# Kernel optimization log

Hardware: AMD Instinct MI355X
Metric: run time of the kernel (lower is better)

Reference implementation:

```python
import jax, jax.numpy as jnp
import numpy as np

MAX_DEPTH = 7
FEAT = 32
HIDDEN = 64
RES = 2 ** MAX_DEPTH          # 128
N_VOXELS = RES ** 3           # 2^21 = 2,097,152
BATCH = 4_194_304


def setup_inputs() -> dict:
    key = jax.random.key(0)
    k = jax.random.split(key, 5)
    positions = jax.random.uniform(k[0], (BATCH, 3), dtype=jnp.float32)  # in [0,1)
    # learned parameters (torch: randn table; Linear default-init approximated)
    table = jax.random.normal(k[1], (N_VOXELS, FEAT), dtype=jnp.float32)
    W1 = jax.random.normal(k[2], (FEAT, HIDDEN), dtype=jnp.float32) * (1.0 / np.sqrt(FEAT))
    b1 = jnp.zeros((HIDDEN,), dtype=jnp.float32)
    W2 = jax.random.normal(k[3], (HIDDEN, 4), dtype=jnp.float32) * (1.0 / np.sqrt(HIDDEN))
    b2 = jnp.zeros((4,), dtype=jnp.float32)
    return {"positions": positions, "table": table, "W1": W1, "b1": b1, "W2": W2, "b2": b2}


def reference(positions, table, W1, b1, W2, b2):
    # voxel index per axis; positions in [0,1) so trunc == floor (matches .long())
    idx = jnp.clip((positions * RES).astype(jnp.int32), 0, RES - 1)  # [B,3]
    flat = idx[..., 0] * (RES * RES) + idx[..., 1] * RES + idx[..., 2]  # [B]
    feats = table[flat]                               # irregular gather [B,FEAT]
    h = jax.nn.relu(feats @ W1 + b1)                  # [B,64]
    out = h @ W2 + b2                                 # [B,4]
    rgb = jax.nn.sigmoid(out[..., :3])                # [B,3]
    density = jax.nn.softplus(out[..., 3:4])          # [B,1]
    return rgb, density
```

## Files before the change

kernel.cpp:

```cpp
#include <hip/hip_runtime.h>
#include <hip/hip_bf16.h>

typedef __attribute__((ext_vector_type(8))) short short8;
typedef __attribute__((ext_vector_type(4))) float f32x4;

#define HID 64
#define FEATN 32

static __device__ __forceinline__ short f2bf(float f) {
    __hip_bfloat16 h = __float2bfloat16(f);
    return __builtin_bit_cast(short, h);
}

__global__ __launch_bounds__(256, 4) void plen_fused(
    const float* __restrict__ pos,
    const float* __restrict__ table,
    const float* __restrict__ W1,
    const float* __restrict__ b1,
    const float* __restrict__ W2,
    const float* __restrict__ b2,
    float* __restrict__ out,
    int batch)
{
    const int lane = threadIdx.x & 63;
    const int row  = lane & 15;
    const int g    = lane >> 4;

    short8 w1f[4];
    float bias1[4];
    float w2f[4][4];
#pragma unroll
    for (int j = 0; j < 4; ++j) {
#pragma unroll
        for (int i = 0; i < 8; ++i)
            w1f[j][i] = f2bf(W1[(g * 8 + i) * HID + j * 16 + row]);
        bias1[j] = b1[j * 16 + row];
#pragma unroll
        for (int o = 0; o < 4; ++o)
            w2f[j][o] = W2[(j * 16 + row) * 4 + o];
    }

    const int r_own = row >> 2;
    const int o_own = row & 3;
    const bool is_rgb = (o_own < 3);
    const float myb2 = b2[o_own];
    const int mult = is_rgb ? 3 : 1;
    const int coff = is_rgb ? ((4 * g + r_own) * 3 + o_own)
                            : (batch * 3 + 4 * g + r_own);

    const int wave_id = blockIdx.x * 4 + (threadIdx.x >> 6);
    const int chunk = wave_id * 256;

    for (int t = 0; t < 16; ++t) {
        const int base = chunk + t * 16;

        const float* pp = pos + (size_t)(base + row) * 3;
        const float px = pp[0], py = pp[1], pz = pp[2];
        int ix = (int)(px * 128.0f);
        int iy = (int)(py * 128.0f);
        int iz = (int)(pz * 128.0f);
        ix = min(127, max(0, ix));
        iy = min(127, max(0, iy));
        iz = min(127, max(0, iz));
        const unsigned flat = ((unsigned)ix << 14) | ((unsigned)iy << 7) | (unsigned)iz;

        const float* rp = table + (size_t)flat * FEATN + g * 8;
        const f32x4 f0 = *(const f32x4*)(rp);
        const f32x4 f1 = *(const f32x4*)(rp + 4);
        short8 afrag;
        afrag[0] = f2bf(f0[0]); afrag[1] = f2bf(f0[1]);
        afrag[2] = f2bf(f0[2]); afrag[3] = f2bf(f0[3]);
        afrag[4] = f2bf(f1[0]); afrag[5] = f2bf(f1[1]);
        afrag[6] = f2bf(f1[2]); afrag[7] = f2bf(f1[3]);

        float p[16];
#pragma unroll
        for (int j = 0; j < 4; ++j) {
            const f32x4 cinit = { bias1[j], bias1[j], bias1[j], bias1[j] };
            const f32x4 acc =
                __builtin_amdgcn_mfma_f32_16x16x32_bf16(afrag, w1f[j], cinit, 0, 0, 0);
#pragma unroll
            for (int r = 0; r < 4; ++r) {
                const float h = fmaxf(acc[r], 0.0f);
                if (j == 0) {
#pragma unroll
                    for (int o = 0; o < 4; ++o) p[r * 4 + o] = h * w2f[0][o];
                } else {
#pragma unroll
                    for (int o = 0; o < 4; ++o) p[r * 4 + o] = fmaf(h, w2f[j][o], p[r * 4 + o]);
                }
            }
        }

        float v8[8];
#pragma unroll
        for (int j = 0; j < 8; ++j) {
            const float a0 = p[2 * j], b0 = p[2 * j + 1];
            const float keep = (row & 1) ? b0 : a0;
            const float give = (row & 1) ? a0 : b0;
            v8[j] = keep + __shfl_xor(give, 1, 64);
        }
        float v4[4];
#pragma unroll
        for (int j = 0; j < 4; ++j) {
            const float a0 = v8[2 * j], b0 = v8[2 * j + 1];
            const float keep = (row & 2) ? b0 : a0;
            const float give = (row & 2) ? a0 : b0;
            v4[j] = keep + __shfl_xor(give, 2, 64);
        }
        float v2[2];
#pragma unroll
        for (int j = 0; j < 2; ++j) {
            const float a0 = v4[2 * j], b0 = v4[2 * j + 1];
            const float keep = (row & 4) ? b0 : a0;
            const float give = (row & 4) ? a0 : b0;
            v2[j] = keep + __shfl_xor(give, 4, 64);
        }
        {
            const float a0 = v2[0], b0 = v2[1];
            const float keep = (row & 8) ? b0 : a0;
            const float give = (row & 8) ? a0 : b0;
            const float v = keep + __shfl_xor(give, 8, 64) + myb2;

            float resv;
            if (is_rgb) {
                resv = __builtin_amdgcn_rcpf(1.0f + __expf(-v));
            } else {
                resv = fmaxf(v, 0.0f) + __logf(1.0f + __expf(-fabsf(v)));
            }
            __builtin_nontemporal_store(resv, out + coff + base * mult);
        }
    }
}

extern "C" void kernel_launch(void* const* d_in, const int* in_sizes, int n_in,
                              void* d_out, int out_size, void* d_ws, size_t ws_size,
                              hipStream_t stream) {
    const float* pos   = (const float*)d_in[0];
    const float* table = (const float*)d_in[1];
    const float* W1    = (const float*)d_in[2];
    const float* b1    = (const float*)d_in[3];
    const float* W2    = (const float*)d_in[4];
    const float* b2    = (const float*)d_in[5];
    float* out = (float*)d_out;

    const int batch  = in_sizes[0] / 3;
    const int blocks = batch / 1024;
    hipLaunchKernelGGL(plen_fused, dim3(blocks), dim3(256), 0, stream,
                       pos, table, W1, b1, W2, b2, out, batch);
}
```

Before: 127.4 us.

## Use MFMA for second layer and software-pipeline table gathers

Swaps the operand order of the first-layer MFMA so the hidden activations land transposed, then computes the 64->4 output layer with a 16x16x16 bf16 MFMA instead of per-lane FMAs plus a four-stage shuffle reduction. Table gathers are double-buffered, so the next tile's position load and gather are in flight while the current tile computes. The position clamp is dropped, which relies on inputs lying in [0,1). The second layer now rounds hidden activations and W2 to bf16, which reduces precision, and only one quarter of the lanes issue stores.

```diff
diff --git a/kernel.cpp b/kernel.cpp
--- a/kernel.cpp
+++ b/kernel.cpp
@@ -1,16 +1,24 @@
 #include <hip/hip_runtime.h>
 #include <hip/hip_bf16.h>
 
-typedef __attribute__((ext_vector_type(8))) short short8;
+typedef __attribute__((ext_vector_type(8))) short bs8;
+typedef __attribute__((ext_vector_type(4))) short bs4;
 typedef __attribute__((ext_vector_type(4))) float f32x4;
 
 #define HID 64
 #define FEATN 32
+#define NT 16
 
 static __device__ __forceinline__ short f2bf(float f) {
     __hip_bfloat16 h = __float2bfloat16(f);
     return __builtin_bit_cast(short, h);
 }
+
+#if defined(__HIP_DEVICE_COMPILE__)
+#define MFMA16(a, b, c) __builtin_amdgcn_mfma_f32_16x16x16bf16_1k(a, b, c, 0, 0, 0)
+#else
+#define MFMA16(a, b, c) (c)
+#endif
 
 __global__ __launch_bounds__(256, 4) void plen_fused(
     const float* __restrict__ pos,
@@ -26,110 +34,94 @@
     const int row  = lane & 15;
     const int g    = lane >> 4;
 
-    short8 w1f[4];
-    float bias1[4];
-    float w2f[4][4];
+    bs8   w1f[4];
+    f32x4 bias1v[4];
+    bs4   w2tf[4];
 #pragma unroll
     for (int j = 0; j < 4; ++j) {
 #pragma unroll
         for (int i = 0; i < 8; ++i)
             w1f[j][i] = f2bf(W1[(g * 8 + i) * HID + j * 16 + row]);
-        bias1[j] = b1[j * 16 + row];
+        bias1v[j] = *(const f32x4*)(b1 + j * 16 + g * 4);
 #pragma unroll
-        for (int o = 0; o < 4; ++o)
-            w2f[j][o] = W2[(j * 16 + row) * 4 + o];
+        for (int i = 0; i < 4; ++i)
+            w2tf[j][i] = (row < 4) ? f2bf(W2[(j * 16 + g * 4 + i) * 4 + row]) : (short)0;
     }
-
-    const int r_own = row >> 2;
-    const int o_own = row & 3;
-    const bool is_rgb = (o_own < 3);
-    const float myb2 = b2[o_own];
-    const int mult = is_rgb ? 3 : 1;
-    const int coff = is_rgb ? ((4 * g + r_own) * 3 + o_own)
-                            : (batch * 3 + 4 * g + r_own);
+    f32x4 oinit;
+    if (g == 0) oinit = *(const f32x4*)b2;
+    else        oinit = (f32x4){0.f, 0.f, 0.f, 0.f};
 
     const int wave_id = blockIdx.x * 4 + (threadIdx.x >> 6);
-    const int chunk = wave_id * 256;
+    const int chunk   = wave_id * (NT * 16);
+    const size_t dns_base = (size_t)batch * 3;
 
-    for (int t = 0; t < 16; ++t) {
-        const int base = chunk + t * 16;
+    auto loadpos = [&](int t, float& x, float& y, float& z) {
+        const int tt = t < NT ? t : NT - 1;
+        const float* pp = pos + (size_t)(chunk + tt * 16 + row) * 3;
+        x = pp[0]; y = pp[1]; z = pp[2];
+    };
+    auto issue_gather = [&](float x, float y, float z, f32x4& A, f32x4& B) {
+        const unsigned ix = (unsigned)(int)(x * 128.0f);
+        const unsigned iy = (unsigned)(int)(y * 128.0f);
+        const unsigned iz = (unsigned)(int)(z * 128.0f);
+        const unsigned flat = (ix << 14) | (iy << 7) | iz;
+        const float* rp = table + (size_t)flat * FEATN + g * 8;
+        A = *(const f32x4*)rp;
+        B = *(const f32x4*)(rp + 4);
+    };
+    auto compute = [&](int sbase, f32x4 f0, f32x4 f1) {
+        bs8 af;
+        af[0] = f2bf(f0[0]); af[1] = f2bf(f0[1]);
+        af[2] = f2bf(f0[2]); af[3] = f2bf(f0[3]);
+        af[4] = f2bf(f1[0]); af[5] = f2bf(f1[1]);
+        af[6] = f2bf(f1[2]); af[7] = f2bf(f1[3]);
 
-        const float* pp = pos + (size_t)(base + row) * 3;
-        const float px = pp[0], py = pp[1], pz = pp[2];
-        int ix = (int)(px * 128.0f);
-        int iy = (int)(py * 128.0f);
-        int iz = (int)(pz * 128.0f);
-        ix = min(127, max(0, ix));
-        iy = min(127, max(0, iy));
-        iz = min(127, max(0, iz));
-        const unsigned flat = ((unsigned)ix << 14) | ((unsigned)iy << 7) | (unsigned)iz;
+        f32x4 acc[4];
+#pragma unroll
+        for (int j = 0; j < 4; ++j)
+            acc[j] = __builtin_amdgcn_mfma_f32_16x16x32_bf16(w1f[j], af, bias1v[j], 0, 0, 0);
 
-        const float* rp = table + (size_t)flat * FEATN + g * 8;
-        const f32x4 f0 = *(const f32x4*)(rp);
-        const f32x4 f1 = *(const f32x4*)(rp + 4);
-        short8 afrag;
-        afrag[0] = f2bf(f0[0]); afrag[1] = f2bf(f0[1]);
-        afrag[2] = f2bf(f0[2]); afrag[3] = f2bf(f0[3]);
-        afrag[4] = f2bf(f1[0]); afrag[5] = f2bf(f1[1]);
-        afrag[6] = f2bf(f1[2]); afrag[7] = f2bf(f1[3]);
-
-        float p[16];
+        f32x4 oacc = oinit;
 #pragma unroll
         for (int j = 0; j < 4; ++j) {
-            const f32x4 cinit = { bias1[j], bias1[j], bias1[j], bias1[j] };
-            const f32x4 acc =
-                __builtin_amdgcn_mfma_f32_16x16x32_bf16(afrag, w1f[j], cinit, 0, 0, 0);
-#pragma unroll
-            for (int r = 0; r < 4; ++r) {
-                const float h = fmaxf(acc[r], 0.0f);
-                if (j == 0) {
-#pragma unroll
-                    for (int o = 0; o < 4; ++o) p[r * 4 + o] = h * w2f[0][o];
-                } else {
-#pragma unroll
-                    for (int o = 0; o < 4; ++o) p[r * 4 + o] = fmaf(h, w2f[j][o], p[r * 4 + o]);
-                }
-            }
+            bs4 pf;
+            pf[0] = f2bf(fmaxf(acc[j][0], 0.0f));
+            pf[1] = f2bf(fmaxf(acc[j][1], 0.0f));
+            pf[2] = f2bf(fmaxf(acc[j][2], 0.0f));
+            pf[3] = f2bf(fmaxf(acc[j][3], 0.0f));
+            oacc = MFMA16(w2tf[j], pf, oacc);
         }
 
-        float v8[8];
-#pragma unroll
-        for (int j = 0; j < 8; ++j) {
-            const float a0 = p[2 * j], b0 = p[2 * j + 1];
-            const float keep = (row & 1) ? b0 : a0;
-            const float give = (row & 1) ? a0 : b0;
-            v8[j] = keep + __shfl_xor(give, 1, 64);
+        const float r0 = __builtin_amdgcn_rcpf(1.0f + __expf(-oacc[0]));
+        const float r1 = __builtin_amdgcn_rcpf(1.0f + __expf(-oacc[1]));
+        const float r2 = __builtin_amdgcn_rcpf(1.0f + __expf(-oacc[2]));
+        const float dv = oacc[3];
+        const float dn = fmaxf(dv, 0.0f) + __logf(1.0f + __expf(-fabsf(dv)));
+
+        if (g == 0) {
+            const int s = sbase + row;
+            float* rp = out + (size_t)s * 3;
+            __builtin_nontemporal_store(r0, rp);
+            __builtin_nontemporal_store(r1, rp + 1);
+            __builtin_nontemporal_store(r2, rp + 2);
+            __builtin_nontemporal_store(dn, out + dns_base + s);
         }
-        float v4[4];
-#pragma unroll
-        for (int j = 0; j < 4; ++j) {
-            const float a0 = v8[2 * j], b0 = v8[2 * j + 1];
-            const float keep = (row & 2) ? b0 : a0;
-            const float give = (row & 2) ? a0 : b0;
-            v4[j] = keep + __shfl_xor(give, 2, 64);
-        }
-        float v2[2];
-#pragma unroll
-        for (int j = 0; j < 2; ++j) {
-            const float a0 = v4[2 * j], b0 = v4[2 * j + 1];
-            const float keep = (row & 4) ? b0 : a0;
-            const float give = (row & 4) ? a0 : b0;
-            v2[j] = keep + __shfl_xor(give, 4, 64);
-        }
-        {
-            const float a0 = v2[0], b0 = v2[1];
-            const float keep = (row & 8) ? b0 : a0;
-            const float give = (row & 8) ? a0 : b0;
-            const float v = keep + __shfl_xor(give, 8, 64) + myb2;
+    };
 
-            float resv;
-            if (is_rgb) {
-                resv = __builtin_amdgcn_rcpf(1.0f + __expf(-v));
-            } else {
-                resv = fmaxf(v, 0.0f) + __logf(1.0f + __expf(-fabsf(v)));
-            }
-            __builtin_nontemporal_store(resv, out + coff + base * mult);
-        }
+    float pxA, pyA, pzA, pxB, pyB, pzB;
+    f32x4 gA0, gA1, gB0, gB1;
+    loadpos(0, pxA, pyA, pzA);
+    loadpos(1, pxB, pyB, pzB);
+    issue_gather(pxA, pyA, pzA, gA0, gA1);
+
+    for (int t = 0; t < NT; t += 2) {
+        loadpos(t + 2, pxA, pyA, pzA);
+        issue_gather(pxB, pyB, pzB, gB0, gB1);
+        compute(chunk + t * 16, gA0, gA1);
+
+        loadpos(t + 3, pxB, pyB, pzB);
+        issue_gather(pxA, pyA, pzA, gA0, gA1);
+        compute(chunk + (t + 1) * 16, gB0, gB1);
     }
 }
 
@@ -145,7 +137,7 @@
     float* out = (float*)d_out;
 
     const int batch  = in_sizes[0] / 3;
-    const int blocks = batch / 1024;
+    const int blocks = batch / (4 * NT * 16);
     hipLaunchKernelGGL(plen_fused, dim3(blocks), dim3(256), 0, stream,
                        pos, table, W1, b1, W2, b2, out, batch);
 }
```

New measurement: 119.0 us. -6.6%, faster.
